# Kernel optimization log

Hardware: AMD Instinct MI355X
Metric: run time of the kernel (lower is better)

## Reference

```python
import jax, jax.numpy as jnp
import numpy as np

EMBED = 64
HEADS = 2
HDIM = EMBED // HEADS  # 32
IN_FEAT = 256
NODES = 3


def _lin(x, W, b=None):
    y = x @ W.T
    return y + b if b is not None else y


def setup_inputs() -> dict:
    key = jax.random.key(0)
    ks = jax.random.split(key, 24)
    B = 131072
    s = 0.05
    inp = {
        "spatial": jax.random.normal(ks[0], (B, IN_FEAT), jnp.float32),
        "genomic": jax.random.normal(ks[1], (B, IN_FEAT), jnp.float32),
        "temporal": jax.random.normal(ks[2], (B, IN_FEAT), jnp.float32),
        "adj_matrix": jnp.ones((B, NODES, NODES), jnp.float32),
        # modality projections (Linear(256,64))
        "Wsp": jax.random.normal(ks[3], (EMBED, IN_FEAT)) * s,
        "bsp": jnp.zeros((EMBED,)),
        "Wge": jax.random.normal(ks[4], (EMBED, IN_FEAT)) * s,
        "bge": jnp.zeros((EMBED,)),
        "Wtm": jax.random.normal(ks[5], (EMBED, IN_FEAT)) * s,
        "btm": jnp.zeros((EMBED,)),
        # GAT: W Linear(64,64,no bias), attention Linear(2*head_dim=64 -> 1, no bias)
        "gat_W": jax.random.normal(ks[6], (EMBED, EMBED)) * s,
        "gat_a": jax.random.normal(ks[7], (2 * HDIM,)) * s,
        # MultiheadAttention(64, 2)
        "in_w": jax.random.normal(ks[8], (3 * EMBED, EMBED)) * s,
        "in_b": jnp.zeros((3 * EMBED,)),
        "out_w": jax.random.normal(ks[9], (EMBED, EMBED)) * s,
        "out_b": jnp.zeros((EMBED,)),
        # LayerNorm(64)
        "ln_g": jnp.ones((EMBED,)),
        "ln_b": jnp.zeros((EMBED,)),
        # predictor 64->32->16->2
        "p1_w": jax.random.normal(ks[10], (32, EMBED)) * s,
        "p1_b": jnp.zeros((32,)),
        "p2_w": jax.random.normal(ks[11], (16, 32)) * s,
        "p2_b": jnp.zeros((16,)),
        "p3_w": jax.random.normal(ks[12], (2, 16)) * s,
        "p3_b": jnp.zeros((2,)),
    }
    return inp


def reference(spatial, genomic, temporal, adj_matrix,
              Wsp, bsp, Wge, bge, Wtm, btm,
              gat_W, gat_a, in_w, in_b, out_w, out_b,
              ln_g, ln_b, p1_w, p1_b, p2_w, p2_b, p3_w, p3_b):
    # Dropout layers are identity in eval mode.
    B = spatial.shape[0]
    sp = jax.nn.relu(_lin(spatial, Wsp, bsp))   # [B, 64]
    ge = jax.nn.relu(_lin(genomic, Wge, bge))
    tm = jax.nn.relu(_lin(temporal, Wtm, btm))
    x = jnp.stack([sp, ge, tm], axis=1)          # [B, 3, 64]

    # ---- GAT layer (dense attention over 3 nodes, 2 heads) ----
    h = _lin(x, gat_W).reshape(B, NODES, HEADS, HDIM)  # [B,3,H,D]
    # a . concat(h_i, h_j) decomposes into a1.h_i + a2.h_j
    e_i = jnp.einsum('bnhd,d->bnh', h, gat_a[:HDIM])
    e_j = jnp.einsum('bnhd,d->bnh', h, gat_a[HDIM:])
    e = e_i[:, :, None, :] + e_j[:, None, :, :]        # [B,3,3,H]
    e = jnp.where(e > 0, e, 0.2 * e)                    # LeakyReLU(0.2)
    e = jnp.where(adj_matrix[..., None] == 0, -1e9, e)
    alpha = jax.nn.softmax(e, axis=2)                   # softmax over j
    h_out = jnp.einsum('bijh,bjhd->bihd', alpha, h).reshape(B, NODES, EMBED)
    gat_pooled = h_out.mean(axis=1)                     # [B, 64]

    # ---- Cross-modal MHA + residual LayerNorm ----
    qkv = _lin(x, in_w, in_b)                           # [B,3,192]
    q, k, v = jnp.split(qkv, 3, axis=-1)
    def heads(t):
        return t.reshape(B, NODES, HEADS, HDIM).transpose(0, 2, 1, 3)
    q, k, v = heads(q), heads(k), heads(v)              # [B,H,3,D]
    sc = jnp.einsum('bhqd,bhkd->bhqk', q, k) / jnp.sqrt(jnp.float32(HDIM))
    attn = jax.nn.softmax(sc, axis=-1)
    o = jnp.einsum('bhqk,bhkd->bhqd', attn, v).transpose(0, 2, 1, 3).reshape(B, NODES, EMBED)
    attn_out = _lin(o, out_w, out_b)
    y = x + attn_out
    mu = y.mean(-1, keepdims=True)
    var = ((y - mu) ** 2).mean(-1, keepdims=True)
    y = (y - mu) / jnp.sqrt(var + 1e-5) * ln_g + ln_b
    cross_modal = y.mean(axis=1)                        # [B, 64]

    # ---- Predictor ----
    combined = gat_pooled + cross_modal
    z = jax.nn.relu(_lin(combined, p1_w, p1_b))
    z = jax.nn.relu(_lin(z, p2_w, p2_b))
    out = _lin(z, p3_w, p3_b)                           # [B, 2]
    return out[:, 0], out[:, 1]
```

## Files before the change

### kernel.cpp

```cpp
#include <hip/hip_runtime.h>

typedef __attribute__((ext_vector_type(8))) short v8s;
typedef __attribute__((ext_vector_type(4))) float v4f;

#define MFMA16(a, b, c) __builtin_amdgcn_mfma_f32_16x16x32_bf16((a), (b), (c), 0, 0, 0)
#define SCQ 0.17677669529663687f

__device__ __forceinline__ short f2bf(float f) {
    unsigned u = __float_as_uint(f);
    u += 0x7FFFu + ((u >> 16) & 1u);
    return (short)(u >> 16);
}
__device__ __forceinline__ float bf2f(short s) {
    return __uint_as_float(((unsigned)(unsigned short)s) << 16);
}
__device__ __forceinline__ float bfly16(float v) {
#pragma unroll
    for (int m = 1; m < 16; m <<= 1) v += __shfl_xor(v, m);
    return v;
}

__global__ void giman_prep(const float* __restrict__ Wsp, const float* __restrict__ Wge,
                           const float* __restrict__ Wtm, const float* __restrict__ gatW,
                           const float* __restrict__ gat_a,
                           const float* __restrict__ inw, const float* __restrict__ outw,
                           const float* __restrict__ p1w, const float* __restrict__ p2w,
                           const float* __restrict__ in_b, const float* __restrict__ out_b,
                           short* __restrict__ ws) {
    int idx = blockIdx.x * 256 + threadIdx.x;
    if (idx < 73216) {
        int j = idx & 7, l = (idx >> 3) & 63;
        int lr = l & 15, lc = ((l >> 4) << 3) + j;
        float val;
        if (idx < 49152) {
            const float* W; int off;
            if (idx < 16384)      { W = Wsp; off = idx; }
            else if (idx < 32768) { W = Wge; off = idx - 16384; }
            else                  { W = Wtm; off = idx - 32768; }
            int t = off >> 9, kk = t & 7, nb = t >> 3;
            val = W[(nb * 16 + lr) * 256 + kk * 32 + lc];
        } else if (idx < 54272) {
            int t = (idx - 49152) >> 9, kk = t & 1, nb = t >> 1;
            if (nb < 4) {
                val = gatW[(nb * 16 + lr) * 64 + kk * 32 + lc];
            } else {
                int f = kk * 32 + lc;
                val = 0.f;
                if (lr < 4) {
                    float s = 0.f;
                    for (int d = 0; d < 32; ++d)
                        s += gat_a[(lr >> 1) * 32 + d] * gatW[((lr & 1) * 32 + d) * 64 + f];
                    val = s;
                } else if (lr < 6) {
                    int h = lr - 4;
                    float s = 0.f;
                    for (int d = 0; d < 32; ++d)
                        s += inw[(32 * h + d) * 64 + f] * in_b[64 + 32 * h + d];
                    val = s * SCQ;
                } else if (lr < 8) {
                    int h = lr - 6;
                    float s = 0.f;
                    for (int d = 0; d < 32; ++d)
                        s += inw[(64 + 32 * h + d) * 64 + f] * in_b[32 * h + d];
                    val = s * SCQ;
                }
            }
        } else if (idx < 62464) {
            int t = (idx - 54272) >> 9, kk = t & 1, nbh = t >> 1;
            int h = nbh >> 2, nb = nbh & 3;
            int a = kk * 32 + lc, b = nb * 16 + lr;
            float s = 0.f;
            for (int d = 0; d < 32; ++d)
                s += inw[(32 * h + d) * 64 + a] * inw[(64 + 32 * h + d) * 64 + b];
            val = s * SCQ;
        } else if (idx < 70656) {
            int t = (idx - 62464) >> 9, kk = t & 1, nbh = t >> 1;
            int h = nbh >> 2, nb = nbh & 3;
            int r = nb * 16 + lr, c = kk * 32 + lc;
            float s = 0.f;
            for (int k = 0; k < 32; ++k)
                s += outw[r * 64 + h * 32 + k] * inw[(128 + h * 32 + k) * 64 + c];
            val = s;
        } else if (idx < 72704) {
            int t = (idx - 70656) >> 9, kk = t & 1, nb = t >> 1;
            val = p1w[(nb * 16 + lr) * 64 + kk * 32 + lc];
        } else {
            val = p2w[lr * 32 + lc];
        }
        ws[idx] = f2bf(val);
    } else if (idx < 73280) {
        int r = idx - 73216;
        float s = out_b[r];
        for (int k = 0; k < 64; ++k) s += outw[r * 64 + 128 + k] * in_b[128 + k];
        ((float*)(ws + 73216))[r] = s;
    } else if (idx < 73282) {
        int h = idx - 73280;
        float s = 0.f;
        for (int d = 0; d < 32; ++d) s += in_b[32 * h + d] * in_b[64 + 32 * h + d];
        ((float*)(ws + 73216))[64 + h] = s * SCQ;
    }
}

__global__ __launch_bounds__(256)
void giman_proj(const float* __restrict__ spatial, const float* __restrict__ genomic,
                const float* __restrict__ temporal,
                const float* __restrict__ bsp, const float* __restrict__ bge,
                const float* __restrict__ btm,
                const short* __restrict__ wf, short* __restrict__ xg, int Btot)
{
    const int wv = threadIdx.x >> 6;
    const int lane = threadIdx.x & 63;
    const int lq = lane & 15, lg = lane >> 4;
    const int nG = Btot >> 6;
    const int nItems = 3 * nG;

    for (int it = blockIdx.x; it < nItems; it += gridDim.x) {
        const int m = it / nG;
        const int g = it - m * nG;
        const int s0 = g * 64 + wv * 16;

        const float* X = (m == 0 ? spatial : (m == 1 ? genomic : temporal))
                       + (size_t)(s0 + lq) * 256 + lg * 8;
        const float* Bm = (m == 0 ? bsp : (m == 1 ? bge : btm));
        const v8s* bwf = (const v8s*)(wf + m * 16384);

        float4 L[16];
#pragma unroll
        for (int k = 0; k < 8; ++k) {
            L[2 * k]     = *(const float4*)(X + k * 32);
            L[2 * k + 1] = *(const float4*)(X + k * 32 + 4);
        }
        __builtin_amdgcn_sched_barrier(0);

        v4f acc[4];
#pragma unroll
        for (int nb = 0; nb < 4; ++nb) acc[nb] = (v4f){0.f, 0.f, 0.f, 0.f};

#pragma unroll
        for (int kk = 0; kk < 8; ++kk) {
            v8s af;
            af[0] = f2bf(L[2 * kk].x); af[1] = f2bf(L[2 * kk].y);
            af[2] = f2bf(L[2 * kk].z); af[3] = f2bf(L[2 * kk].w);
            af[4] = f2bf(L[2 * kk + 1].x); af[5] = f2bf(L[2 * kk + 1].y);
            af[6] = f2bf(L[2 * kk + 1].z); af[7] = f2bf(L[2 * kk + 1].w);
#pragma unroll
            for (int nb = 0; nb < 4; ++nb)
                acc[nb] = MFMA16(af, bwf[(nb * 8 + kk) * 64 + lane], acc[nb]);
        }

        float bb0 = Bm[lq], bb1 = Bm[16 + lq], bb2 = Bm[32 + lq], bb3 = Bm[48 + lq];
#pragma unroll
        for (int nb = 0; nb < 4; ++nb) {
            float bb = nb == 0 ? bb0 : (nb == 1 ? bb1 : (nb == 2 ? bb2 : bb3));
#pragma unroll
            for (int r = 0; r < 4; ++r) {
                float v = acc[nb][r] + bb;
                v = v > 0.f ? v : 0.f;
                xg[((size_t)(s0 + 4 * lg + r) * 3 + m) * 64 + nb * 16 + lq] = f2bf(v);
            }
        }
    }
}

__global__ __launch_bounds__(256)
void giman_main(const float* __restrict__ adj, const short* __restrict__ wf,
                const short* __restrict__ xg,
                const float* __restrict__ ln_g, const float* __restrict__ ln_b,
                const float* __restrict__ p1b, const float* __restrict__ p2b,
                const float* __restrict__ p3w, const float* __restrict__ p3bb,
                float* __restrict__ dout, int Btot)
{
    __shared__ __align__(16) short x_lds[4][48][72];
    __shared__ __align__(16) short v_lds[4][16][72];
    __shared__ __align__(16) float a_lds[4][148];

    const int wv   = threadIdx.x >> 6;
    const int lane = threadIdx.x & 63;
    const int lq   = lane & 15;
    const int lg   = lane >> 4;
    const int grpb = lane & 48;
    const int s0   = blockIdx.x * 64 + wv * 16;
    if (s0 + 16 > Btot) return;

    short (*xw)[72] = x_lds[wv];
    short (*vtr)[72] = v_lds[wv];

    if (lane < 36)
        *(float4*)&a_lds[wv][lane * 4] = *(const float4*)(adj + (size_t)s0 * 9 + lane * 4);

    {
        const short* xsrc = xg + (size_t)s0 * 192;
#pragma unroll
        for (int i = 0; i < 6; ++i) {
            int c = lane + 64 * i;
            v8s val = *(const v8s*)(xsrc + c * 8);
            *(v8s*)&xw[c >> 3][(c & 7) * 8] = val;
        }
    }

    const float* cbp = (const float*)(wf + 73216);
    float cbv[4], lgv[4], lbv[4];
#pragma unroll
    for (int nb = 0; nb < 4; ++nb) {
        int c = nb * 16 + lq;
        cbv[nb] = cbp[c];
        lgv[nb] = ln_g[c];
        lbv[nb] = ln_b[c];
    }
    const float gmv0 = cbp[64], gmv1 = cbp[65];
    const float inv3 = 1.f / 3.f;

    const v8s* gwf = (const v8s*)(wf + 49152);
    const v8s* pff = (const v8s*)(wf + 54272);
    const v8s* uf  = (const v8s*)(wf + 62464);

#pragma unroll 1
    for (int t = 0; t < 4; ++t) {
        int rn = lq & 3; rn = (rn == 3) ? 2 : rn;
        const short* xrp = xw[(t * 4 + (lq >> 2)) * 3 + rn];
        v8s xa0 = *(const v8s*)(xrp + lg * 8);
        v8s xa1 = *(const v8s*)(xrp + 32 + lg * 8);

        float gp[4];
        v4f eacc = (v4f){0.f, 0.f, 0.f, 0.f};
        {
            v4f hacc[4];
#pragma unroll
            for (int nb = 0; nb < 4; ++nb) {
                v4f a = (v4f){0.f, 0.f, 0.f, 0.f};
                a = MFMA16(xa0, gwf[(nb * 2 + 0) * 64 + lane], a);
                a = MFMA16(xa1, gwf[(nb * 2 + 1) * 64 + lane], a);
                hacc[nb] = a;
            }
            eacc = MFMA16(xa0, gwf[8 * 64 + lane], eacc);
            eacc = MFMA16(xa1, gwf[9 * 64 + lane], eacc);

            const float* amp = &a_lds[wv][(t * 4 + lg) * 9];
            float wj0[2], wj1[2], wj2[2];
#pragma unroll
            for (int h = 0; h < 2; ++h) {
                float ei0 = __shfl(eacc[0], grpb + h);
                float ei1 = __shfl(eacc[1], grpb + h);
                float ei2 = __shfl(eacc[2], grpb + h);
                float ej0 = __shfl(eacc[0], grpb + 2 + h);
                float ej1 = __shfl(eacc[1], grpb + 2 + h);
                float ej2 = __shfl(eacc[2], grpb + 2 + h);
                float w0 = 0.f, w1 = 0.f, w2 = 0.f;
#pragma unroll
                for (int i = 0; i < 3; ++i) {
                    float eiv = i == 0 ? ei0 : (i == 1 ? ei1 : ei2);
                    float e0 = eiv + ej0; e0 = e0 > 0.f ? e0 : 0.2f * e0; if (amp[i * 3 + 0] == 0.f) e0 = -1e9f;
                    float e1 = eiv + ej1; e1 = e1 > 0.f ? e1 : 0.2f * e1; if (amp[i * 3 + 1] == 0.f) e1 = -1e9f;
                    float e2 = eiv + ej2; e2 = e2 > 0.f ? e2 : 0.2f * e2; if (amp[i * 3 + 2] == 0.f) e2 = -1e9f;
                    float mx = fmaxf(e0, fmaxf(e1, e2));
                    float q0 = __expf(e0 - mx), q1 = __expf(e1 - mx), q2 = __expf(e2 - mx);
                    float inv = 1.f / (q0 + q1 + q2);
                    w0 += q0 * inv; w1 += q1 * inv; w2 += q2 * inv;
                }
                wj0[h] = w0; wj1[h] = w1; wj2[h] = w2;
            }
#pragma unroll
            for (int nb = 0; nb < 4; ++nb) {
                int h = nb >> 1;
                gp[nb] = (wj0[h] * hacc[nb][0] + wj1[h] * hacc[nb][1] + wj2[h] * hacc[nb][2]) * inv3;
            }
        }

        float y[4][3];
#pragma unroll
        for (int nb = 0; nb < 4; ++nb)
#pragma unroll
            for (int r = 0; r < 3; ++r)
                y[nb][r] = bf2f(xw[(t * 4 + lg) * 3 + r][nb * 16 + lq]) + cbv[nb];

        const int sb = grpb + (grpb >> 2);
#pragma unroll
        for (int h = 0; h < 2; ++h) {
            {
                v4f va[4];
#pragma unroll
                for (int nb = 0; nb < 4; ++nb) {
                    v4f a = (v4f){0.f, 0.f, 0.f, 0.f};
                    a = MFMA16(xa0, pff[((h * 4 + nb) * 2 + 0) * 64 + lane], a);
                    a = MFMA16(xa1, pff[((h * 4 + nb) * 2 + 1) * 64 + lane], a);
                    va[nb] = a;
                }
#pragma unroll
                for (int nb = 0; nb < 4; ++nb)
#pragma unroll
                    for (int r = 0; r < 3; ++r)
                        vtr[lg * 4 + r][nb * 16 + lq] = f2bf(va[nb][r]);
            }
            v8s aq0 = *(const v8s*)&vtr[lq][lg * 8];
            v8s aq1 = *(const v8s*)&vtr[lq][32 + lg * 8];
            v4f S = (v4f){0.f, 0.f, 0.f, 0.f};
            S = MFMA16(aq0, xa0, S);
            S = MFMA16(aq1, xa1, S);

            float alh[9];
            {
                float gm = h ? gmv1 : gmv0;
                float bv0 = __shfl(eacc[0], grpb + 6 + h) + gm;
                float bv1 = __shfl(eacc[1], grpb + 6 + h) + gm;
                float bv2 = __shfl(eacc[2], grpb + 6 + h) + gm;
#pragma unroll
                for (int i = 0; i < 3; ++i) {
                    float av = __shfl(eacc[i], grpb + 4 + h);
                    float e0 = __shfl(S[i], sb + 0) + av + bv0;
                    float e1 = __shfl(S[i], sb + 1) + av + bv1;
                    float e2 = __shfl(S[i], sb + 2) + av + bv2;
                    float mx = fmaxf(e0, fmaxf(e1, e2));
                    float w0 = __expf(e0 - mx), w1 = __expf(e1 - mx), w2 = __expf(e2 - mx);
                    float inv = 1.f / (w0 + w1 + w2);
                    alh[i * 3 + 0] = w0 * inv;
                    alh[i * 3 + 1] = w1 * inv;
                    alh[i * 3 + 2] = w2 * inv;
                }
            }

#pragma unroll
            for (int nb = 0; nb < 4; ++nb) {
                v4f u = (v4f){0.f, 0.f, 0.f, 0.f};
                u = MFMA16(xa0, uf[((h * 4 + nb) * 2 + 0) * 64 + lane], u);
                u = MFMA16(xa1, uf[((h * 4 + nb) * 2 + 1) * 64 + lane], u);
#pragma unroll
                for (int r = 0; r < 3; ++r)
                    y[nb][r] += alh[r * 3 + 0] * u[0] + alh[r * 3 + 1] * u[1]
                              + alh[r * 3 + 2] * u[2];
            }
        }

        float mu[3], rs[3];
#pragma unroll
        for (int r = 0; r < 3; ++r) {
            float sm = y[0][r] + y[1][r] + y[2][r] + y[3][r];
            float sq = y[0][r] * y[0][r] + y[1][r] * y[1][r]
                     + y[2][r] * y[2][r] + y[3][r] * y[3][r];
            sm = bfly16(sm); sq = bfly16(sq);
            float m_ = sm * (1.f / 64.f);
            float var = sq * (1.f / 64.f) - m_ * m_;
            mu[r] = m_;
            rs[r] = rsqrtf(var + 1e-5f);
        }
#pragma unroll
        for (int nb = 0; nb < 4; ++nb) {
            float cm = (y[nb][0] - mu[0]) * rs[0] + (y[nb][1] - mu[1]) * rs[1]
                     + (y[nb][2] - mu[2]) * rs[2];
            float comb = gp[nb] + cm * inv3 * lgv[nb] + lbv[nb];
            xw[t * 4 + lg][nb * 16 + lq] = f2bf(comb);
        }
    }

    {
        const v8s* p1f = (const v8s*)(wf + 70656);
        const v8s* p2f = (const v8s*)(wf + 72704);
        short (*zw)[40] = (short (*)[40])(&xw[16][0]);
        const short* crp = &xw[lq][0];
        v8s ca0 = *(const v8s*)(crp + lg * 8);
        v8s ca1 = *(const v8s*)(crp + 32 + lg * 8);
        const float pb1v0 = p1b[lq], pb1v1 = p1b[16 + lq], pb2v = p2b[lq];
        const float p3w0 = p3w[lq], p3w1 = p3w[16 + lq];
        v4f z1[2];
#pragma unroll
        for (int nb = 0; nb < 2; ++nb) {
            float bb = nb ? pb1v1 : pb1v0;
            v4f a = (v4f){bb, bb, bb, bb};
            a = MFMA16(ca0, p1f[(nb * 2 + 0) * 64 + lane], a);
            a = MFMA16(ca1, p1f[(nb * 2 + 1) * 64 + lane], a);
            z1[nb] = a;
        }
#pragma unroll
        for (int nb = 0; nb < 2; ++nb)
#pragma unroll
            for (int r = 0; r < 4; ++r) {
                float v = z1[nb][r];
                v = v > 0.f ? v : 0.f;
                zw[lg * 4 + r][nb * 16 + lq] = f2bf(v);
            }
        v8s za = *(const v8s*)(&zw[lq][0] + lg * 8);
        v4f z2 = (v4f){pb2v, pb2v, pb2v, pb2v};
        z2 = MFMA16(za, p2f[lane], z2);
        const float p3b0 = p3bb[0], p3b1 = p3bb[1];
#pragma unroll
        for (int r = 0; r < 4; ++r) {
            float v = z2[r];
            v = v > 0.f ? v : 0.f;
            float po0 = bfly16(v * p3w0);
            float po1 = bfly16(v * p3w1);
            if (lq == 0) {
                dout[s0 + lg * 4 + r] = po0 + p3b0;
                dout[Btot + s0 + lg * 4 + r] = po1 + p3b1;
            }
        }
    }
}

extern "C" void kernel_launch(void* const* d_in, const int* in_sizes, int n_in,
                              void* d_out, int out_size, void* d_ws, size_t ws_size,
                              hipStream_t stream) {
    const float* spatial  = (const float*)d_in[0];
    const float* genomic  = (const float*)d_in[1];
    const float* temporal = (const float*)d_in[2];
    const float* adj      = (const float*)d_in[3];
    const float* Wsp = (const float*)d_in[4];
    const float* bsp = (const float*)d_in[5];
    const float* Wge = (const float*)d_in[6];
    const float* bge = (const float*)d_in[7];
    const float* Wtm = (const float*)d_in[8];
    const float* btm = (const float*)d_in[9];
    const float* gatW  = (const float*)d_in[10];
    const float* gat_a = (const float*)d_in[11];
    const float* in_w  = (const float*)d_in[12];
    const float* in_b  = (const float*)d_in[13];
    const float* out_w = (const float*)d_in[14];
    const float* out_b = (const float*)d_in[15];
    const float* ln_g  = (const float*)d_in[16];
    const float* ln_b  = (const float*)d_in[17];
    const float* p1w = (const float*)d_in[18];
    const float* p1b = (const float*)d_in[19];
    const float* p2w = (const float*)d_in[20];
    const float* p2b = (const float*)d_in[21];
    const float* p3w = (const float*)d_in[22];
    const float* p3b = (const float*)d_in[23];
    float* out = (float*)d_out;
    const int Btot = in_sizes[0] / 256;

    short* wf = (short*)d_ws;
    short* xg = wf + 81920;

    giman_prep<<<(73282 + 255) / 256, 256, 0, stream>>>(Wsp, Wge, Wtm, gatW, gat_a,
                                                        in_w, out_w, p1w, p2w,
                                                        in_b, out_b, wf);
    giman_proj<<<2048, 256, 0, stream>>>(spatial, genomic, temporal,
                                         bsp, bge, btm, wf, xg, Btot);
    giman_main<<<Btot / 64, 256, 0, stream>>>(adj, wf, xg,
                                              ln_g, ln_b, p1b, p2b, p3w, p3b,
                                              out, Btot);
}
```

Measured before the change: 225.0 us.

## Stage projection inputs through LDS with global_load_lds and per-wave work items

The projection kernel now copies each 16-row input tile into a padded per-wave LDS buffer using global_load_lds, with fully coalesced 1 KB row loads. It then reads bf16 MFMA fragments from LDS instead of holding strided float4 loads in registers. Work is handed out per wave (16-row items) rather than per block, and the grid drops from 2048 to 512 blocks. This aims to improve global load coalescing and cut register pressure. In exchange it uses about 66 KB of LDS per block, which limits occupancy, and it waits on vmcnt(0) with no double buffering, so memory latency may be poorly hidden.

```diff
diff --git a/kernel.cpp b/kernel.cpp
--- a/kernel.cpp
+++ b/kernel.cpp
@@ -18,6 +18,10 @@
 #pragma unroll
     for (int m = 1; m < 16; m <<= 1) v += __shfl_xor(v, m);
     return v;
+}
+__device__ __forceinline__ void gload16(const float* g, float* l) {
+    __builtin_amdgcn_global_load_lds((const __attribute__((address_space(1))) void*)g,
+                                     (__attribute__((address_space(3))) void*)l, 16, 0, 0);
 }
 
 __global__ void giman_prep(const float* __restrict__ Wsp, const float* __restrict__ Wge,
@@ -108,50 +112,53 @@
                 const float* __restrict__ btm,
                 const short* __restrict__ wf, short* __restrict__ xg, int Btot)
 {
+    __shared__ __align__(16) float xs[4][16][260];
+
     const int wv = threadIdx.x >> 6;
     const int lane = threadIdx.x & 63;
     const int lq = lane & 15, lg = lane >> 4;
-    const int nG = Btot >> 6;
+    float* buf = &xs[wv][0][0];
+
+    const int nG = Btot >> 4;
     const int nItems = 3 * nG;
-
-    for (int it = blockIdx.x; it < nItems; it += gridDim.x) {
+    const int wid = blockIdx.x * 4 + wv;
+    const int wstride = gridDim.x * 4;
+
+    for (int it = wid; it < nItems; it += wstride) {
         const int m = it / nG;
         const int g = it - m * nG;
-        const int s0 = g * 64 + wv * 16;
-
-        const float* X = (m == 0 ? spatial : (m == 1 ? genomic : temporal))
-                       + (size_t)(s0 + lq) * 256 + lg * 8;
-        const float* Bm = (m == 0 ? bsp : (m == 1 ? bge : btm));
+        const float* Xm = (m == 0 ? spatial : (m == 1 ? genomic : temporal));
+        const float* src = Xm + (size_t)g * 16 * 256;
+
+#pragma unroll
+        for (int i = 0; i < 16; ++i)
+            gload16(src + i * 256 + lane * 4, buf + i * 260);
+        asm volatile("s_waitcnt vmcnt(0)" ::: "memory");
+        __builtin_amdgcn_sched_barrier(0);
+
         const v8s* bwf = (const v8s*)(wf + m * 16384);
-
-        float4 L[16];
-#pragma unroll
-        for (int k = 0; k < 8; ++k) {
-            L[2 * k]     = *(const float4*)(X + k * 32);
-            L[2 * k + 1] = *(const float4*)(X + k * 32 + 4);
-        }
-        __builtin_amdgcn_sched_barrier(0);
-
         v4f acc[4];
 #pragma unroll
         for (int nb = 0; nb < 4; ++nb) acc[nb] = (v4f){0.f, 0.f, 0.f, 0.f};
 
 #pragma unroll
         for (int kk = 0; kk < 8; ++kk) {
+            const float* rp = buf + lq * 260 + kk * 32 + lg * 8;
+            float4 u = *(const float4*)rp;
+            float4 v = *(const float4*)(rp + 4);
             v8s af;
-            af[0] = f2bf(L[2 * kk].x); af[1] = f2bf(L[2 * kk].y);
-            af[2] = f2bf(L[2 * kk].z); af[3] = f2bf(L[2 * kk].w);
-            af[4] = f2bf(L[2 * kk + 1].x); af[5] = f2bf(L[2 * kk + 1].y);
-            af[6] = f2bf(L[2 * kk + 1].z); af[7] = f2bf(L[2 * kk + 1].w);
+            af[0] = f2bf(u.x); af[1] = f2bf(u.y); af[2] = f2bf(u.z); af[3] = f2bf(u.w);
+            af[4] = f2bf(v.x); af[5] = f2bf(v.y); af[6] = f2bf(v.z); af[7] = f2bf(v.w);
 #pragma unroll
             for (int nb = 0; nb < 4; ++nb)
                 acc[nb] = MFMA16(af, bwf[(nb * 8 + kk) * 64 + lane], acc[nb]);
         }
 
-        float bb0 = Bm[lq], bb1 = Bm[16 + lq], bb2 = Bm[32 + lq], bb3 = Bm[48 + lq];
+        const float* Bm = (m == 0 ? bsp : (m == 1 ? bge : btm));
+        const int s0 = g * 16;
 #pragma unroll
         for (int nb = 0; nb < 4; ++nb) {
-            float bb = nb == 0 ? bb0 : (nb == 1 ? bb1 : (nb == 2 ? bb2 : bb3));
+            float bb = Bm[nb * 16 + lq];
 #pragma unroll
             for (int r = 0; r < 4; ++r) {
                 float v = acc[nb][r] + bb;
@@ -431,8 +438,8 @@
     giman_prep<<<(73282 + 255) / 256, 256, 0, stream>>>(Wsp, Wge, Wtm, gatW, gat_a,
                                                         in_w, out_w, p1w, p2w,
                                                         in_b, out_b, wf);
-    giman_proj<<<2048, 256, 0, stream>>>(spatial, genomic, temporal,
-                                         bsp, bge, btm, wf, xg, Btot);
+    giman_proj<<<512, 256, 0, stream>>>(spatial, genomic, temporal,
+                                        bsp, bge, btm, wf, xg, Btot);
     giman_main<<<Btot / 64, 256, 0, stream>>>(adj, wf, xg,
                                               ln_g, ln_b, p1b, p2b, p3w, p3b,
                                               out, Btot);
```

Measured after the change: 285.3 us. +26.8%, slower.
